# Kernel tuning notes

Measured on AMD Instinct MI355X. Metric: run time of the kernel, lower is better.

## Reference

```python
import jax, jax.numpy as jnp
import numpy as np

DIN = 4096
DOUT = 12288
NUM_GATES = DOUT // 3
OFFSET = 1
BS = 4096
Z = 1.0

# fixed 3x5 combine matrix from the module
M = jnp.array([[1., 0., 0., 0., 0.],
               [0., 0., 1., 1., -1.],
               [0., 1., 0., -1., 1.]], dtype=jnp.float32)


def _make_connections():
    g = np.arange(NUM_GATES, dtype=np.int64)
    starts = (g * 3 + OFFSET) % DIN
    conn = (starts[:, None] + np.arange(3, dtype=np.int64)[None, :]) % DIN
    return jnp.asarray(conn, dtype=jnp.int32)


def setup_inputs() -> dict:
    key = jax.random.key(0)
    kx, kw = jax.random.split(key)
    x = jax.random.normal(kx, (BS, DIN), dtype=jnp.float32)
    wgts = jax.random.normal(kw, (NUM_GATES, 3, 4), dtype=jnp.float32)
    connections = _make_connections()
    return {"x": x, "wgts": wgts, "connections": connections}


def reference(x, wgts, connections):
    bs = x.shape[0]
    # gather 3 inputs per gate: [bs, G, 3]
    gathered = x[:, connections]
    # append constant z -> [bs, G, 4]
    zcol = jnp.full((bs, NUM_GATES, 1), Z, dtype=x.dtype)
    inp = jnp.concatenate([gathered, zcol], axis=-1)
    # softmax-weighted small matmul (training path): [G,3,4] x [bs,G,4] -> [bs,G,3]
    wp = jax.nn.softmax(wgts, axis=-1)
    s = jnp.einsum('gik,bgk->bgi', wp, inp)
    # elementwise products -> [bs, G, 5]
    v4 = s[..., 0] * s[..., 1]
    v5 = s[..., 0] * s[..., 2]
    feats = jnp.concatenate([s, v4[..., None], v5[..., None]], axis=-1)
    # fixed 3x5 combine: [bs, G, 3]
    signals = jnp.einsum('rk,bgk->bgr', M, feats)
    # strided slice ::3 on last dim (size 3) keeps only index 0 -> [bs, G]
    out = signals[:, :, ::3].reshape(bs, -1)
    return out
```

## Files before the change

kernel.cpp:

```cpp
#include <hip/hip_runtime.h>

#define DIN 4096
#define NG  4096
#define BS  4096
#define RPB 8
#define BT  1024

typedef float v4f __attribute__((ext_vector_type(4)));

__global__ __launch_bounds__(BT, 4) void fredkin_s0_stream(
    const float* __restrict__ x,
    const float* __restrict__ wgts,
    float* __restrict__ out)
{
    const int tid = threadIdx.x;
    const int l   = tid & 63;
    const int g0  = 4 * tid;

    float4 wq[4];
#pragma unroll
    for (int j = 0; j < 4; ++j) {
        float4 r = *reinterpret_cast<const float4*>(wgts + (size_t)(g0 + j) * 12);
        float m  = fmaxf(fmaxf(r.x, r.y), fmaxf(r.z, r.w));
        float e0 = __expf(r.x - m);
        float e1 = __expf(r.y - m);
        float e2 = __expf(r.z - m);
        float e3 = __expf(r.w - m);
        float inv = 1.0f / (e0 + e1 + e2 + e3);
        wq[j] = make_float4(e0 * inv, e1 * inv, e2 * inv, e3 * inv);
    }

    const int brow = blockIdx.x * RPB;
    const float* xb   = x   + (size_t)brow * DIN;
    float*       orow = out + (size_t)brow * NG + g0;

    const int lb = (12 * tid) & (DIN - 1);
    const int i1 = (lb + 4)  & (DIN - 1);
    const int i2 = (lb + 8)  & (DIN - 1);
    const int i3 = (lb + 12) & (DIN - 1);

#pragma unroll
    for (int r = 0; r < RPB; ++r) {
        const float* xr = xb + (size_t)r * DIN;
        float4 f0 = *reinterpret_cast<const float4*>(xr + lb);
        float4 f1 = *reinterpret_cast<const float4*>(xr + i1);
        float4 f2 = *reinterpret_cast<const float4*>(xr + i2);
        float e12 = __shfl_down(f0.x, 1);
        if (l == 63) e12 = xr[i3];
        v4f o;
        o.x = fmaf(wq[0].x, f0.y, fmaf(wq[0].y, f0.z, fmaf(wq[0].z, f0.w, wq[0].w)));
        o.y = fmaf(wq[1].x, f1.x, fmaf(wq[1].y, f1.y, fmaf(wq[1].z, f1.z, wq[1].w)));
        o.z = fmaf(wq[2].x, f1.w, fmaf(wq[2].y, f2.x, fmaf(wq[2].z, f2.y, wq[2].w)));
        o.w = fmaf(wq[3].x, f2.z, fmaf(wq[3].y, f2.w, fmaf(wq[3].z, e12, wq[3].w)));
        __builtin_nontemporal_store(o, reinterpret_cast<v4f*>(orow + (size_t)r * NG));
    }
}

extern "C" void kernel_launch(void* const* d_in, const int* in_sizes, int n_in,
                              void* d_out, int out_size, void* d_ws, size_t ws_size,
                              hipStream_t stream) {
    const float* x    = (const float*)d_in[0];
    const float* wgts = (const float*)d_in[1];
    float* out = (float*)d_out;

    fredkin_s0_stream<<<dim3(BS / RPB), dim3(BT), 0, stream>>>(x, wgts, out);
}
```

Before: 127.2 us.

## Split blocks into 256-thread gate groups and software-prefetch next row

Shrinks the block from 1024 to 256 threads and splits each 8-row tile across four blocks by gate group, so the grid is four times larger. It also double-buffers the x loads, fetching row r+1 while row r is computed and stored. The aim is more scheduling flexibility and more loads in flight to hide memory latency. In exchange, each block recomputes the softmax for its own gates and register pressure goes up. Since the loop is fully unrolled, the compiler may already have hoisted the loads, so the prefetch may change little.

```diff
diff --git a/kernel.cpp b/kernel.cpp
--- a/kernel.cpp
+++ b/kernel.cpp
@@ -4,18 +4,22 @@
 #define NG  4096
 #define BS  4096
 #define RPB 8
-#define BT  1024
+#define BT  256
+#define GG  4
 
 typedef float v4f __attribute__((ext_vector_type(4)));
 
-__global__ __launch_bounds__(BT, 4) void fredkin_s0_stream(
+__global__ __launch_bounds__(BT, 8) void fredkin_s0_ilp(
     const float* __restrict__ x,
     const float* __restrict__ wgts,
     float* __restrict__ out)
 {
     const int tid = threadIdx.x;
     const int l   = tid & 63;
-    const int g0  = 4 * tid;
+    const int gg  = blockIdx.x & (GG - 1);
+    const int rg  = blockIdx.x >> 2;
+    const int gq  = (gg << 8) + tid;
+    const int g0  = gq << 2;
 
     float4 wq[4];
 #pragma unroll
@@ -30,29 +34,48 @@
         wq[j] = make_float4(e0 * inv, e1 * inv, e2 * inv, e3 * inv);
     }
 
-    const int brow = blockIdx.x * RPB;
+    const int brow = rg * RPB;
     const float* xb   = x   + (size_t)brow * DIN;
     float*       orow = out + (size_t)brow * NG + g0;
 
-    const int lb = (12 * tid) & (DIN - 1);
+    const int lb = (12 * gq) & (DIN - 1);
     const int i1 = (lb + 4)  & (DIN - 1);
     const int i2 = (lb + 8)  & (DIN - 1);
     const int i3 = (lb + 12) & (DIN - 1);
 
+    float4 a0, a1, a2;
+    float  as;
+    {
+        const float* xr = xb;
+        a0 = *reinterpret_cast<const float4*>(xr + lb);
+        a1 = *reinterpret_cast<const float4*>(xr + i1);
+        a2 = *reinterpret_cast<const float4*>(xr + i2);
+        as = (l == 63) ? xr[i3] : 0.0f;
+    }
+
 #pragma unroll
     for (int r = 0; r < RPB; ++r) {
-        const float* xr = xb + (size_t)r * DIN;
-        float4 f0 = *reinterpret_cast<const float4*>(xr + lb);
-        float4 f1 = *reinterpret_cast<const float4*>(xr + i1);
-        float4 f2 = *reinterpret_cast<const float4*>(xr + i2);
-        float e12 = __shfl_down(f0.x, 1);
-        if (l == 63) e12 = xr[i3];
+        float4 b0 = {}, b1 = {}, b2 = {};
+        float  bs_ = 0.0f;
+        if (r + 1 < RPB) {
+            const float* xn = xb + (size_t)(r + 1) * DIN;
+            b0 = *reinterpret_cast<const float4*>(xn + lb);
+            b1 = *reinterpret_cast<const float4*>(xn + i1);
+            b2 = *reinterpret_cast<const float4*>(xn + i2);
+            bs_ = (l == 63) ? xn[i3] : 0.0f;
+        }
+
+        float e12 = __shfl_down(a0.x, 1);
+        if (l == 63) e12 = as;
+
         v4f o;
-        o.x = fmaf(wq[0].x, f0.y, fmaf(wq[0].y, f0.z, fmaf(wq[0].z, f0.w, wq[0].w)));
-        o.y = fmaf(wq[1].x, f1.x, fmaf(wq[1].y, f1.y, fmaf(wq[1].z, f1.z, wq[1].w)));
-        o.z = fmaf(wq[2].x, f1.w, fmaf(wq[2].y, f2.x, fmaf(wq[2].z, f2.y, wq[2].w)));
-        o.w = fmaf(wq[3].x, f2.z, fmaf(wq[3].y, f2.w, fmaf(wq[3].z, e12, wq[3].w)));
+        o.x = fmaf(wq[0].x, a0.y, fmaf(wq[0].y, a0.z, fmaf(wq[0].z, a0.w, wq[0].w)));
+        o.y = fmaf(wq[1].x, a1.x, fmaf(wq[1].y, a1.y, fmaf(wq[1].z, a1.z, wq[1].w)));
+        o.z = fmaf(wq[2].x, a1.w, fmaf(wq[2].y, a2.x, fmaf(wq[2].z, a2.y, wq[2].w)));
+        o.w = fmaf(wq[3].x, a2.z, fmaf(wq[3].y, a2.w, fmaf(wq[3].z, e12, wq[3].w)));
         __builtin_nontemporal_store(o, reinterpret_cast<v4f*>(orow + (size_t)r * NG));
+
+        a0 = b0; a1 = b1; a2 = b2; as = bs_;
     }
 }
 
@@ -63,5 +86,5 @@
     const float* wgts = (const float*)d_in[1];
     float* out = (float*)d_out;
 
-    fredkin_s0_stream<<<dim3(BS / RPB), dim3(BT), 0, stream>>>(x, wgts, out);
+    fredkin_s0_ilp<<<dim3((BS / RPB) * GG), dim3(BT), 0, stream>>>(x, wgts, out);
 }
```

New measurement: 138.2 us. 8.7% more time.

## Stage x rows in LDS via global_load_lds DMA and compute gates from shared memory

Applied to the files above, without the earlier changes.

Each block now copies two full input rows into LDS with asynchronous global-to-LDS loads, padding the row with its first 64 elements so wrapped gate indices resolve. Each thread then computes eight gates per row from LDS with scalar nontemporal stores. This removes the shuffle and boundary handling and aims for fully coalesced x reads. In exchange, per-block softmax of weights is amortized over far fewer rows, which increases redundant weight reads and exp work, and stores become scalar.

```diff
diff --git a/kernel.cpp b/kernel.cpp
--- a/kernel.cpp
+++ b/kernel.cpp
@@ -1,58 +1,81 @@
 #include <hip/hip_runtime.h>
 
-#define DIN 4096
-#define NG  4096
-#define BS  4096
-#define RPB 8
-#define BT  1024
+#define DIN  4096
+#define NG   4096
+#define BS   4096
+#define R    2
+#define BT   512
+#define GPT  8
+#define PAD  64
+#define ROWF (DIN + PAD)
 
-typedef float v4f __attribute__((ext_vector_type(4)));
+__device__ __forceinline__ void dma16(const float* g, float* lds) {
+    __builtin_amdgcn_global_load_lds(
+        (const __attribute__((address_space(1))) void*)g,
+        (__attribute__((address_space(3))) void*)lds, 16, 0, 0);
+}
+__device__ __forceinline__ void dma4(const float* g, float* lds) {
+    __builtin_amdgcn_global_load_lds(
+        (const __attribute__((address_space(1))) void*)g,
+        (__attribute__((address_space(3))) void*)lds, 4, 0, 0);
+}
 
-__global__ __launch_bounds__(BT, 4) void fredkin_s0_stream(
+__global__ __launch_bounds__(BT, 8) void fredkin_rows(
     const float* __restrict__ x,
     const float* __restrict__ wgts,
     float* __restrict__ out)
 {
+    __shared__ float L[R][ROWF];
+
     const int tid = threadIdx.x;
+    const int w   = tid >> 6;
     const int l   = tid & 63;
-    const int g0  = 4 * tid;
+    const int row0 = blockIdx.x * R;
 
-    float4 wq[4];
 #pragma unroll
-    for (int j = 0; j < 4; ++j) {
-        float4 r = *reinterpret_cast<const float4*>(wgts + (size_t)(g0 + j) * 12);
-        float m  = fmaxf(fmaxf(r.x, r.y), fmaxf(r.z, r.w));
-        float e0 = __expf(r.x - m);
-        float e1 = __expf(r.y - m);
-        float e2 = __expf(r.z - m);
-        float e3 = __expf(r.w - m);
-        float inv = 1.0f / (e0 + e1 + e2 + e3);
-        wq[j] = make_float4(e0 * inv, e1 * inv, e2 * inv, e3 * inv);
+    for (int r = 0; r < R; ++r) {
+        const float* xr = x + (size_t)(row0 + r) * DIN;
+        float* Lr = &L[r][0];
+        dma16(xr + (w << 9) + (l << 2),       Lr + (w << 9));
+        dma16(xr + (w << 9) + 256 + (l << 2), Lr + (w << 9) + 256);
+    }
+    if (w < R) {
+        const float* xr = x + (size_t)(row0 + w) * DIN;
+        dma4(xr + l, &L[w][DIN]);
     }
 
-    const int brow = blockIdx.x * RPB;
-    const float* xb   = x   + (size_t)brow * DIN;
-    float*       orow = out + (size_t)brow * NG + g0;
+    float4 wq[GPT];
+#pragma unroll
+    for (int k = 0; k < GPT; ++k) {
+        const int g = tid + (k << 9);
+        float4 rr = *reinterpret_cast<const float4*>(wgts + (size_t)g * 12);
+        float m  = fmaxf(fmaxf(rr.x, rr.y), fmaxf(rr.z, rr.w));
+        float e0 = __expf(rr.x - m);
+        float e1 = __expf(rr.y - m);
+        float e2 = __expf(rr.z - m);
+        float e3 = __expf(rr.w - m);
+        float inv = 1.0f / (e0 + e1 + e2 + e3);
+        wq[k] = make_float4(e0 * inv, e1 * inv, e2 * inv, e3 * inv);
+    }
 
-    const int lb = (12 * tid) & (DIN - 1);
-    const int i1 = (lb + 4)  & (DIN - 1);
-    const int i2 = (lb + 8)  & (DIN - 1);
-    const int i3 = (lb + 12) & (DIN - 1);
+    __syncthreads();
 
+    const int t3 = 3 * tid;
 #pragma unroll
-    for (int r = 0; r < RPB; ++r) {
-        const float* xr = xb + (size_t)r * DIN;
-        float4 f0 = *reinterpret_cast<const float4*>(xr + lb);
-        float4 f1 = *reinterpret_cast<const float4*>(xr + i1);
-        float4 f2 = *reinterpret_cast<const float4*>(xr + i2);
-        float e12 = __shfl_down(f0.x, 1);
-        if (l == 63) e12 = xr[i3];
-        v4f o;
-        o.x = fmaf(wq[0].x, f0.y, fmaf(wq[0].y, f0.z, fmaf(wq[0].z, f0.w, wq[0].w)));
-        o.y = fmaf(wq[1].x, f1.x, fmaf(wq[1].y, f1.y, fmaf(wq[1].z, f1.z, wq[1].w)));
-        o.z = fmaf(wq[2].x, f1.w, fmaf(wq[2].y, f2.x, fmaf(wq[2].z, f2.y, wq[2].w)));
-        o.w = fmaf(wq[3].x, f2.z, fmaf(wq[3].y, f2.w, fmaf(wq[3].z, e12, wq[3].w)));
-        __builtin_nontemporal_store(o, reinterpret_cast<v4f*>(orow + (size_t)r * NG));
+    for (int r = 0; r < R; ++r) {
+        const float* Lr = &L[r][0];
+        float* orow = out + (size_t)(row0 + r) * NG;
+#pragma unroll
+        for (int k = 0; k < GPT; ++k) {
+            const int jb = (t3 + k * 1536) & (DIN - 1);
+            float e1 = Lr[jb + 1];
+            float e2 = Lr[jb + 2];
+            float e3 = Lr[jb + 3];
+            float o = fmaf(wq[k].x, e1,
+                      fmaf(wq[k].y, e2,
+                      fmaf(wq[k].z, e3, wq[k].w)));
+            __builtin_nontemporal_store(o, orow + tid + (k << 9));
+        }
     }
 }
 
@@ -63,5 +86,5 @@
     const float* wgts = (const float*)d_in[1];
     float* out = (float*)d_out;
 
-    fredkin_s0_stream<<<dim3(BS / RPB), dim3(BT), 0, stream>>>(x, wgts, out);
+    fredkin_rows<<<dim3(BS / R), dim3(BT), 0, stream>>>(x, wgts, out);
 }
```

Measured after the change: 121.1 us. -4.8%, faster.

## Stream rows through per-wave LDS double buffers with direct global-to-LDS loads

Applied to the files above, without the earlier changes.

Each wave now owns a contiguous slice of 256 gates. It stages the corresponding 769 input floats of each row into a private LDS buffer using global_load_lds DMA, double-buffering across rows with explicit vmcnt waits. Rows per block double to 16, and outputs are written as scalar nontemporal stores instead of float4. The aim is to overlap the load of the next row with compute on the current one and to remove the cross-lane shuffle. In exchange it uses about 106 KB of LDS per block, which limits occupancy, and it relies on hand-tuned waitcnt values and scalar stores.

```diff
diff --git a/kernel.cpp b/kernel.cpp
--- a/kernel.cpp
+++ b/kernel.cpp
@@ -1,59 +1,112 @@
 #include <hip/hip_runtime.h>
 
-#define DIN 4096
-#define NG  4096
-#define BS  4096
-#define RPB 8
-#define BT  1024
+#define DIN  4096
+#define NG   4096
+#define BS   4096
+#define RPB  16
+#define BT   1024
+#define NW   16
+#define WFL  832
 
-typedef float v4f __attribute__((ext_vector_type(4)));
+#define WAITVM(N) __builtin_amdgcn_s_waitcnt((N) | 0x0F70)
 
-__global__ __launch_bounds__(BT, 4) void fredkin_s0_stream(
+__device__ __forceinline__ void dma16(const float* g, float* lds) {
+    __builtin_amdgcn_global_load_lds(
+        (const __attribute__((address_space(1))) void*)g,
+        (__attribute__((address_space(3))) void*)lds, 16, 0, 0);
+}
+__device__ __forceinline__ void dma4(const float* g, float* lds) {
+    __builtin_amdgcn_global_load_lds(
+        (const __attribute__((address_space(1))) void*)g,
+        (__attribute__((address_space(3))) void*)lds, 4, 0, 0);
+}
+
+__global__ __launch_bounds__(BT, 4) void fredkin_wavepriv(
     const float* __restrict__ x,
     const float* __restrict__ wgts,
     float* __restrict__ out)
 {
+    __shared__ float E[NW][WFL];
+    __shared__ float O[NW][WFL];
+
     const int tid = threadIdx.x;
+    const int v   = tid >> 6;
     const int l   = tid & 63;
-    const int g0  = 4 * tid;
+    const int row0 = blockIdx.x * RPB;
 
     float4 wq[4];
 #pragma unroll
-    for (int j = 0; j < 4; ++j) {
-        float4 r = *reinterpret_cast<const float4*>(wgts + (size_t)(g0 + j) * 12);
+    for (int k = 0; k < 4; ++k) {
+        const int g = (v << 8) + l + (k << 6);
+        float4 r = *reinterpret_cast<const float4*>(wgts + (size_t)g * 12);
         float m  = fmaxf(fmaxf(r.x, r.y), fmaxf(r.z, r.w));
         float e0 = __expf(r.x - m);
         float e1 = __expf(r.y - m);
         float e2 = __expf(r.z - m);
         float e3 = __expf(r.w - m);
         float inv = 1.0f / (e0 + e1 + e2 + e3);
-        wq[j] = make_float4(e0 * inv, e1 * inv, e2 * inv, e3 * inv);
+        wq[k] = make_float4(e0 * inv, e1 * inv, e2 * inv, e3 * inv);
     }
 
-    const int brow = blockIdx.x * RPB;
-    const float* xb   = x   + (size_t)brow * DIN;
-    float*       orow = out + (size_t)brow * NG + g0;
+    const int wb = 3 * (v << 8);
+    const int s0 = (wb       + (l << 2)) & (DIN - 1);
+    const int s1 = (wb + 256 + (l << 2)) & (DIN - 1);
+    const int s2 = (wb + 512 + (l << 2)) & (DIN - 1);
+    const int s3 = (wb + 768 +  l      ) & (DIN - 1);
+    float* We = &E[v][0];
+    float* Wo = &O[v][0];
 
-    const int lb = (12 * tid) & (DIN - 1);
-    const int i1 = (lb + 4)  & (DIN - 1);
-    const int i2 = (lb + 8)  & (DIN - 1);
-    const int i3 = (lb + 12) & (DIN - 1);
+#define STAGE(DST, R_) {                                              \
+        const float* xr = x + (size_t)(row0 + (R_)) * DIN;            \
+        dma16(xr + s0, (DST));                                        \
+        dma16(xr + s1, (DST) + 256);                                  \
+        dma16(xr + s2, (DST) + 512);                                  \
+        dma4 (xr + s3, (DST) + 768);                                  \
+    }
 
-#pragma unroll
-    for (int r = 0; r < RPB; ++r) {
-        const float* xr = xb + (size_t)r * DIN;
-        float4 f0 = *reinterpret_cast<const float4*>(xr + lb);
-        float4 f1 = *reinterpret_cast<const float4*>(xr + i1);
-        float4 f2 = *reinterpret_cast<const float4*>(xr + i2);
-        float e12 = __shfl_down(f0.x, 1);
-        if (l == 63) e12 = xr[i3];
-        v4f o;
-        o.x = fmaf(wq[0].x, f0.y, fmaf(wq[0].y, f0.z, fmaf(wq[0].z, f0.w, wq[0].w)));
-        o.y = fmaf(wq[1].x, f1.x, fmaf(wq[1].y, f1.y, fmaf(wq[1].z, f1.z, wq[1].w)));
-        o.z = fmaf(wq[2].x, f1.w, fmaf(wq[2].y, f2.x, fmaf(wq[2].z, f2.y, wq[2].w)));
-        o.w = fmaf(wq[3].x, f2.z, fmaf(wq[3].y, f2.w, fmaf(wq[3].z, e12, wq[3].w)));
-        __builtin_nontemporal_store(o, reinterpret_cast<v4f*>(orow + (size_t)r * NG));
+    asm volatile("" ::: "memory");
+    STAGE(We, 0)
+
+    const int t1 = 3 * l + 1;
+
+#define FRED_ITER(R_, NWAIT, CUR, NXT, DO_STAGE)                              \
+    {                                                                         \
+        if (DO_STAGE) STAGE(NXT, (R_) + 1)                                    \
+        asm volatile("" ::: "memory");                                        \
+        WAITVM(NWAIT);                                                        \
+        asm volatile("" ::: "memory");                                        \
+        float* orow = out + (size_t)(row0 + (R_)) * NG + (v << 8) + l;        \
+        _Pragma("unroll")                                                     \
+        for (int k = 0; k < 4; ++k) {                                         \
+            const float* p = (CUR) + t1 + 192 * k;                            \
+            float e1 = p[0];                                                  \
+            float e2 = p[1];                                                  \
+            float e3 = p[2];                                                  \
+            float o = fmaf(wq[k].x, e1,                                       \
+                      fmaf(wq[k].y, e2,                                       \
+                      fmaf(wq[k].z, e3, wq[k].w)));                           \
+            __builtin_nontemporal_store(o, orow + (k << 6));                  \
+        }                                                                     \
     }
+
+    FRED_ITER( 0, 4, We, Wo, 1)
+    FRED_ITER( 1, 8, Wo, We, 1)
+    FRED_ITER( 2, 8, We, Wo, 1)
+    FRED_ITER( 3, 8, Wo, We, 1)
+    FRED_ITER( 4, 8, We, Wo, 1)
+    FRED_ITER( 5, 8, Wo, We, 1)
+    FRED_ITER( 6, 8, We, Wo, 1)
+    FRED_ITER( 7, 8, Wo, We, 1)
+    FRED_ITER( 8, 8, We, Wo, 1)
+    FRED_ITER( 9, 8, Wo, We, 1)
+    FRED_ITER(10, 8, We, Wo, 1)
+    FRED_ITER(11, 8, Wo, We, 1)
+    FRED_ITER(12, 8, We, Wo, 1)
+    FRED_ITER(13, 8, Wo, We, 1)
+    FRED_ITER(14, 8, We, Wo, 1)
+    FRED_ITER(15, 4, Wo, We, 0)
+#undef FRED_ITER
+#undef STAGE
 }
 
 extern "C" void kernel_launch(void* const* d_in, const int* in_sizes, int n_in,
@@ -63,5 +116,5 @@
     const float* wgts = (const float*)d_in[1];
     float* out = (float*)d_out;
 
-    fredkin_s0_stream<<<dim3(BS / RPB), dim3(BT), 0, stream>>>(x, wgts, out);
+    fredkin_wavepriv<<<dim3(BS / RPB), dim3(BT), 0, stream>>>(x, wgts, out);
 }
```

New measurement: 129.8 us. +2.1%, slower.
